# Optimization experiments

Hardware: AMD Instinct MI355X
Metric: run time of the kernel (lower is better)

The kernel has to match this reference:

```python
import jax, jax.numpy as jnp
import numpy as np

E = 1024  # embed_dim
H = 16    # num_heads
D = E // H  # head_dim
B, S = 2, 2048


def setup_inputs() -> dict:
    key = jax.random.key(0)
    ks = jax.random.split(key, 8)
    q = jax.random.normal(ks[0], (B, S, E), dtype=jnp.float32)
    k = jax.random.normal(ks[1], (B, S, E), dtype=jnp.float32)
    v = jax.random.normal(ks[2], (B, S, E), dtype=jnp.float32)
    mask = jax.random.randint(ks[3], (1, 1, S, S), 0, 2, dtype=jnp.int32)
    sc = 1.0 / np.sqrt(E)
    Wqkv = jax.random.normal(ks[4], (E, 3 * E), dtype=jnp.float32) * sc  # [in, out]
    bqkv = jnp.zeros((3 * E,), dtype=jnp.float32)
    Wout = jax.random.normal(ks[5], (E, E), dtype=jnp.float32) * sc
    bout = jnp.zeros((E,), dtype=jnp.float32)
    return {"q": q, "k": k, "v": v, "mask": mask,
            "Wqkv": Wqkv, "bqkv": bqkv, "Wout": Wout, "bout": bout}


def reference(q, k, v, mask, Wqkv, bqkv, Wout, bout):
    # Fused QKV projection: project cat([q,k,v], dim=0) with the shared 3E proj,
    # then take the Q slice for q, K slice for k, V slice for v.
    x = jnp.concatenate([q, k, v], axis=0)            # [3B, S, E]
    full = jnp.einsum('bse,ef->bsf', x, Wqkv) + bqkv  # [3B, S, 3E]
    qf, kf, vf = jnp.split(full, 3, axis=0)           # each [B, S, 3E]
    qh = qf[..., :E].reshape(B, S, H, D).transpose(0, 2, 1, 3)       # [B,H,S,D]
    kh = kf[..., E:2 * E].reshape(B, S, H, D).transpose(0, 2, 1, 3)
    vh = vf[..., 2 * E:].reshape(B, S, H, D).transpose(0, 2, 1, 3)
    scores = jnp.einsum('bhqd,bhkd->bhqk', qh, kh) / np.sqrt(D)      # [B,H,S,S]
    scores = jnp.where(mask == 0, -jnp.inf, scores)
    attn = jax.nn.softmax(scores, axis=-1)
    ctx = jnp.einsum('bhqk,bhkd->bhqd', attn, vh)                    # [B,H,S,D]
    ctx = ctx.transpose(0, 2, 1, 3).reshape(B, S, E)
    return jnp.einsum('bse,ef->bsf', ctx, Wout) + bout
```

## Files before the change

### kernel.cpp

```cpp
#include <hip/hip_runtime.h>
#include <stdint.h>

#define EDIM 1024
#define HNUM 16
#define HD   64
#define BB   2
#define SS   2048
#define MTOT (BB * SS)

typedef __attribute__((ext_vector_type(8))) __bf16 bf16x8;
typedef __attribute__((ext_vector_type(8))) short short8;
typedef __attribute__((ext_vector_type(4))) short short4v;
typedef __attribute__((ext_vector_type(4))) float f32x4;

__device__ __forceinline__ short bfbits(float f) {
  __bf16 h = (__bf16)f;
  return __builtin_bit_cast(short, h);
}

__device__ __forceinline__ void gload16(const void* g, void* l) {
  __builtin_amdgcn_global_load_lds((const __attribute__((address_space(1))) void*)g,
                                   (__attribute__((address_space(3))) void*)l, 16, 0, 0);
}

__device__ __forceinline__ int kap_perm(int k) {
  return (k & 0x20) | ((k & 0xC) << 1) | ((k & 0x10) >> 2) | (k & 3);
}

__global__ __launch_bounds__(256) void prep(
    const float* __restrict__ q, const float* __restrict__ k,
    const float* __restrict__ v, const float* __restrict__ Wqkv,
    const float* __restrict__ Wout, const int* __restrict__ mask,
    short* __restrict__ Qb, short* __restrict__ Kb, short* __restrict__ Vb,
    short* __restrict__ WqT, short* __restrict__ WkT, short* __restrict__ WvT,
    short* __restrict__ WoT, unsigned long long* __restrict__ pm) {
  __shared__ short L[64][80];
  const int bid = blockIdx.x, t = threadIdx.x;

  if (bid < 6144) {
    const int which = bid >> 11;
    const int i = (bid & 2047) * 256 + t;
    const float* s = which == 0 ? q : (which == 1 ? k : v);
    short* d = which == 0 ? Qb : (which == 1 ? Kb : Vb);
    const float4* sp = (const float4*)s + (size_t)i * 2;
    float4 a = sp[0], b = sp[1];
    short8 r;
    r[0] = bfbits(a.x); r[1] = bfbits(a.y); r[2] = bfbits(a.z); r[3] = bfbits(a.w);
    r[4] = bfbits(b.x); r[5] = bfbits(b.y); r[6] = bfbits(b.z); r[7] = bfbits(b.w);
    *(short8*)(d + (size_t)i * 8) = r;
  } else if (bid < 7168) {
    const int tb = bid - 6144;
    const int which = tb >> 8;
    const int k0 = ((tb >> 4) & 15) * 64, n0 = (tb & 15) * 64;
    const float* W = which == 3 ? Wout : Wqkv;
    const int ld = which == 3 ? EDIM : 3 * EDIM;
    const int col0 = which == 3 ? 0 : which * EDIM;
    short* D = which == 0 ? WqT : (which == 1 ? WkT : (which == 2 ? WvT : WoT));
    {
      const int kr = t >> 2, nc0 = (t & 3) * 16;
      #pragma unroll
      for (int u = 0; u < 4; ++u) {
        float4 f = *(const float4*)(W + (size_t)(k0 + kr) * ld + col0 + n0 + nc0 + u * 4);
        L[nc0 + u * 4 + 0][kr] = bfbits(f.x);
        L[nc0 + u * 4 + 1][kr] = bfbits(f.y);
        L[nc0 + u * 4 + 2][kr] = bfbits(f.z);
        L[nc0 + u * 4 + 3][kr] = bfbits(f.w);
      }
    }
    __syncthreads();
    {
      const int nr = t >> 2, kc = (t & 3) * 16;
      #pragma unroll
      for (int u = 0; u < 2; ++u) {
        short8 vv = *(const short8*)&L[nr][kc + u * 8];
        *(short8*)(D + (size_t)(n0 + nr) * EDIM + k0 + kc + u * 8) = vv;
      }
    }
  } else {
    const int wid = (bid - 7168) * 4 + (t >> 6);
    const int lane = t & 63;
    const int qq = wid >> 5, kt = wid & 31;
    const int m = mask[(size_t)qq * SS + kt * 64 + lane];
    const unsigned long long b = __ballot(m != 0);
    if (lane == 0) pm[(size_t)qq * 32 + kt] = b;
  }
}

template <int NFR, int MODE, typename OT>
__device__ __forceinline__ void gemm_body(
    const short* __restrict__ A, const short* __restrict__ Bt,
    const float* __restrict__ bias, OT* __restrict__ O,
    int m0, int n0, int K, int N, float scale, short* As, short* Bs) {
  const int t = threadIdx.x;
  const int w = t >> 6, l = t & 63;
  const int wr = w >> 1, wc = w & 1;
  const int lr4 = l >> 4, lc = l & 15;

  f32x4 acc[4][NFR] = {};
  const int srow = t >> 3;
  const int schunk = (t & 7) ^ (srow & 7);

  for (int k0 = 0; k0 < K; k0 += 64) {
    #pragma unroll
    for (int p = 0; p < 4; ++p)
      gload16(A + (size_t)(m0 + 32 * p + srow) * K + k0 + schunk * 8,
              As + p * 2048 + w * 512);
    #pragma unroll
    for (int p = 0; p < NFR; ++p)
      gload16(Bt + (size_t)(n0 + 32 * p + srow) * K + k0 + schunk * 8,
              Bs + p * 2048 + w * 512);
    __syncthreads();

    #pragma unroll
    for (int kf = 0; kf < 2; ++kf) {
      const int c = ((4 * kf + lr4) ^ (lc & 7)) * 8;
      bf16x8 a[4], bfr[NFR];
      #pragma unroll
      for (int i = 0; i < 4; ++i)
        a[i] = *(const bf16x8*)(As + (64 * wr + 16 * i + lc) * 64 + c);
      #pragma unroll
      for (int j = 0; j < NFR; ++j)
        bfr[j] = *(const bf16x8*)(Bs + (16 * NFR * wc + 16 * j + lc) * 64 + c);
      #pragma unroll
      for (int i = 0; i < 4; ++i)
        #pragma unroll
        for (int j = 0; j < NFR; ++j)
          acc[i][j] = __builtin_amdgcn_mfma_f32_16x16x32_bf16(a[i], bfr[j], acc[i][j], 0, 0, 0);
    }
    __syncthreads();
  }

  #pragma unroll
  for (int j = 0; j < NFR; ++j) {
    const int col = n0 + 16 * NFR * wc + 16 * j + lc;
    const float bv = bias[col];
    #pragma unroll
    for (int i = 0; i < 4; ++i) {
      const int rbase = m0 + 64 * wr + 16 * i + 4 * lr4;
      if constexpr (MODE == 2) {
        const int bidx = rbase >> 11, s = rbase & 2047;
        const int hh = col >> 6, dd = col & 63;
        short4v o;
        #pragma unroll
        for (int r = 0; r < 4; ++r) o[r] = bfbits((acc[i][j][r] + bv) * scale);
        *(short4v*)((short*)O + (((size_t)bidx * HNUM + hh) * 64 + dd) * SS +
                    (s & ~63) + kap_perm(s & 63)) = o;
      } else {
        #pragma unroll
        for (int r = 0; r < 4; ++r) {
          float vv = (acc[i][j][r] + bv) * scale;
          if constexpr (MODE == 0)
            ((short*)O)[(size_t)(rbase + r) * N + col] = bfbits(vv);
          else
            ((float*)O)[(size_t)(rbase + r) * N + col] = vv;
        }
      }
    }
  }
}

__global__ __launch_bounds__(256) void gemm_qkv(
    const short* __restrict__ Qb, const short* __restrict__ Kb,
    const short* __restrict__ Vb, const short* __restrict__ WqT,
    const short* __restrict__ WkT, const short* __restrict__ WvT,
    const float* __restrict__ bqkv, short* __restrict__ Qpj,
    short* __restrict__ Kpj, short* __restrict__ VT) {
  __shared__ short As[128 * 64];
  __shared__ short Bs[128 * 64];
  const int sel = blockIdx.y >> 3;
  const int n0 = (blockIdx.y & 7) * 128;
  const int m0 = blockIdx.x * 128;
  if (sel == 0)
    gemm_body<4, 0, short>(Qb, WqT, bqkv, Qpj, m0, n0, EDIM, EDIM,
                           0.125f * 1.44269504089f, As, Bs);
  else if (sel == 1)
    gemm_body<4, 0, short>(Kb, WkT, bqkv + EDIM, Kpj, m0, n0, EDIM, EDIM,
                           1.0f, As, Bs);
  else
    gemm_body<4, 2, short>(Vb, WvT, bqkv + 2 * EDIM, VT, m0, n0, EDIM, EDIM,
                           1.0f, As, Bs);
}

__global__ __launch_bounds__(256) void gemm_out(
    const short* __restrict__ A, const short* __restrict__ Bt,
    const float* __restrict__ bias, float* __restrict__ O) {
  __shared__ short As[128 * 64];
  __shared__ short Bs[64 * 64];
  gemm_body<2, 1, float>(A, Bt, bias, O, blockIdx.x * 128, blockIdx.y * 64,
                         EDIM, EDIM, 1.0f, As, Bs);
}

__global__ __launch_bounds__(256) void attn_mfma(
    const short* __restrict__ Qp, const short* __restrict__ Kp,
    const short* __restrict__ VT, const unsigned long long* __restrict__ pmask,
    short* __restrict__ Ctx) {
  __shared__ short Ks[2][64 * 64];
  __shared__ short Vt[2][64 * 64];

  const int t = threadIdx.x, w = t >> 6, l = t & 63;
  const int lr4 = l >> 4, lc = l & 15;
  const int q0 = blockIdx.x * 64;
  const int h = blockIdx.y, b = blockIdx.z;
  const size_t hb = (size_t)b * SS * EDIM + (size_t)h * HD;
  const size_t hv = ((size_t)b * HNUM + h) * 64 * SS;
  const int qrow = q0 + 16 * w + lc;

  bf16x8 qf[2];
  #pragma unroll
  for (int kf = 0; kf < 2; ++kf)
    qf[kf] = *(const bf16x8*)(Qp + hb + (size_t)qrow * EDIM + 32 * kf + 8 * lr4);

  const int srow = t >> 3;
  const int schunk = (t & 7) ^ (srow & 7);

  #pragma unroll
  for (int p = 0; p < 2; ++p) {
    gload16(Kp + hb + (size_t)(32 * p + srow) * EDIM + schunk * 8,
            &Ks[0][p * 2048 + w * 512]);
    gload16(VT + hv + (size_t)(32 * p + srow) * SS + schunk * 8,
            &Vt[0][p * 2048 + w * 512]);
  }
  __syncthreads();

  f32x4 accO[4] = {};
  float mrow = -1e30f, lrow = 0.f;
  const int NT = SS / 64;

  for (int kt = 0; kt < NT; ++kt) {
    const int cur = kt & 1, nxt = cur ^ 1;
    const unsigned long long pw = pmask[(size_t)qrow * NT + kt];
    if (kt + 1 < NT) {
      const size_t sK = hb + (size_t)((kt + 1) * 64) * EDIM;
      const size_t sV = hv + (size_t)((kt + 1) * 64);
      #pragma unroll
      for (int p = 0; p < 2; ++p) {
        gload16(Kp + sK + (size_t)(32 * p + srow) * EDIM + schunk * 8,
                &Ks[nxt][p * 2048 + w * 512]);
        gload16(VT + sV + (size_t)(32 * p + srow) * SS + schunk * 8,
                &Vt[nxt][p * 2048 + w * 512]);
      }
    }

    f32x4 sacc[4] = {};
    #pragma unroll
    for (int kf = 0; kf < 2; ++kf) {
      const int c = ((4 * kf + lr4) ^ (lc & 7)) * 8;
      #pragma unroll
      for (int nf = 0; nf < 4; ++nf) {
        bf16x8 kb8 = *(const bf16x8*)(&Ks[cur][(16 * nf + lc) * 64 + c]);
        sacc[nf] = __builtin_amdgcn_mfma_f32_16x16x32_bf16(kb8, qf[kf], sacc[nf], 0, 0, 0);
      }
    }

    float mt = -1e30f;
    #pragma unroll
    for (int nf = 0; nf < 4; ++nf)
      #pragma unroll
      for (int r = 0; r < 4; ++r)
        mt = fmaxf(mt, sacc[nf][r]);
    mt = fmaxf(mt, __shfl_xor(mt, 16, 64));
    mt = fmaxf(mt, __shfl_xor(mt, 32, 64));

    if (__any(mt > mrow + 7.0f)) {
      const float mn = fmaxf(mrow, mt);
      const float scl = exp2f(mrow - mn);
      mrow = mn;
      lrow *= scl;
      #pragma unroll
      for (int df = 0; df < 4; ++df)
        #pragma unroll
        for (int r = 0; r < 4; ++r)
          accO[df][r] *= scl;
    }

    float ls = 0.f;
    bf16x8 pf[2];
    #pragma unroll
    for (int nf = 0; nf < 4; ++nf) {
      const unsigned nib = (unsigned)(pw >> (16 * nf + 4 * lr4)) & 15u;
      #pragma unroll
      for (int r = 0; r < 4; ++r) {
        const float e = exp2f(sacc[nf][r] - mrow);
        const float p = (nib >> r) & 1u ? e : 0.f;
        ls += p;
        pf[nf >> 1][4 * (nf & 1) + r] = (__bf16)p;
      }
    }
    ls += __shfl_xor(ls, 16, 64);
    ls += __shfl_xor(ls, 32, 64);
    lrow += ls;

    #pragma unroll
    for (int kf = 0; kf < 2; ++kf) {
      const int c = ((4 * kf + lr4) ^ (lc & 7)) * 8;
      #pragma unroll
      for (int df = 0; df < 4; ++df) {
        bf16x8 va = *(const bf16x8*)(&Vt[cur][(16 * df + lc) * 64 + c]);
        accO[df] = __builtin_amdgcn_mfma_f32_16x16x32_bf16(va, pf[kf], accO[df], 0, 0, 0);
      }
    }
    __syncthreads();
  }

  const float inv = 1.f / lrow;
  #pragma unroll
  for (int df = 0; df < 4; ++df) {
    short4v o;
    #pragma unroll
    for (int r = 0; r < 4; ++r) o[r] = bfbits(accO[df][r] * inv);
    *(short4v*)(Ctx + hb + (size_t)qrow * EDIM + 16 * df + 4 * lr4) = o;
  }
}

extern "C" void kernel_launch(void* const* d_in, const int* in_sizes, int n_in,
                              void* d_out, int out_size, void* d_ws, size_t ws_size,
                              hipStream_t stream) {
  const float* q    = (const float*)d_in[0];
  const float* k    = (const float*)d_in[1];
  const float* v    = (const float*)d_in[2];
  const int*   mask = (const int*)d_in[3];
  const float* Wqkv = (const float*)d_in[4];
  const float* bqkv = (const float*)d_in[5];
  const float* Wout = (const float*)d_in[6];
  const float* bout = (const float*)d_in[7];
  float* out = (float*)d_out;

  const size_t mat = (size_t)MTOT * EDIM;
  const size_t wmat = (size_t)EDIM * EDIM;
  short* Qb  = (short*)d_ws;
  short* Kb  = Qb + mat;
  short* Vb  = Kb + mat;
  short* WqT = Vb + mat;
  short* WkT = WqT + wmat;
  short* WvT = WkT + wmat;
  short* WoT = WvT + wmat;
  short* Qpj = WoT + wmat;
  short* Kpj = Qpj + mat;
  short* VT  = Kpj + mat;
  short* Ctx = VT + mat;
  unsigned long long* pm = (unsigned long long*)(Ctx + mat);

  prep<<<dim3(23552), 256, 0, stream>>>(q, k, v, Wqkv, Wout, mask,
                                        Qb, Kb, Vb, WqT, WkT, WvT, WoT, pm);

  gemm_qkv<<<dim3(MTOT / 128, 24), 256, 0, stream>>>(Qb, Kb, Vb, WqT, WkT, WvT,
                                                     bqkv, Qpj, Kpj, VT);

  attn_mfma<<<dim3(SS / 64, HNUM, BB), 256, 0, stream>>>(Qpj, Kpj, VT, pm, Ctx);

  gemm_out<<<dim3(MTOT / 128, EDIM / 64), 256, 0, stream>>>(Ctx, WoT, bout, out);
}
```

Baseline: 267.8 us.

## Switch attention to 32x32x16 MFMA with two waves per block

The attention kernel moves from 16x16x32 to 32x32x16 bf16 MFMA tiles, so each wave owns 32 query rows and the block shrinks from four waves to two. The V-transpose permutation written by the QKV GEMM and the packed-mask bit indexing are reworked to match the new accumulator lane layout. The larger tiles aim to cut LDS reads and shuffle reductions per FLOP, at the cost of fewer waves per block and more registers per lane.

```diff
diff --git a/kernel.cpp b/kernel.cpp
--- a/kernel.cpp
+++ b/kernel.cpp
@@ -12,6 +12,7 @@
 typedef __attribute__((ext_vector_type(8))) short short8;
 typedef __attribute__((ext_vector_type(4))) short short4v;
 typedef __attribute__((ext_vector_type(4))) float f32x4;
+typedef __attribute__((ext_vector_type(16))) float f32x16;
 
 __device__ __forceinline__ short bfbits(float f) {
   __bf16 h = (__bf16)f;
@@ -23,8 +24,8 @@
                                    (__attribute__((address_space(3))) void*)l, 16, 0, 0);
 }
 
-__device__ __forceinline__ int kap_perm(int k) {
-  return (k & 0x20) | ((k & 0xC) << 1) | ((k & 0x10) >> 2) | (k & 3);
+__device__ __forceinline__ int sigma_perm(int k) {
+  return (k & ~0xC) | ((k & 4) << 1) | ((k & 8) >> 1);
 }
 
 __global__ __launch_bounds__(256) void prep(
@@ -144,7 +145,7 @@
         #pragma unroll
         for (int r = 0; r < 4; ++r) o[r] = bfbits((acc[i][j][r] + bv) * scale);
         *(short4v*)((short*)O + (((size_t)bidx * HNUM + hh) * 64 + dd) * SS +
-                    (s & ~63) + kap_perm(s & 63)) = o;
+                    (s & ~63) + sigma_perm(s & 63)) = o;
       } else {
         #pragma unroll
         for (int r = 0; r < 4; ++r) {
@@ -190,75 +191,82 @@
                          EDIM, EDIM, 1.0f, As, Bs);
 }
 
-__global__ __launch_bounds__(256) void attn_mfma(
+__global__ __launch_bounds__(128) void attn_mfma(
     const short* __restrict__ Qp, const short* __restrict__ Kp,
     const short* __restrict__ VT, const unsigned long long* __restrict__ pmask,
     short* __restrict__ Ctx) {
-  __shared__ short Ks[2][64 * 64];
-  __shared__ short Vt[2][64 * 64];
+  __shared__ short Ks[2][4096];
+  __shared__ short Vt[2][4096];
 
   const int t = threadIdx.x, w = t >> 6, l = t & 63;
-  const int lr4 = l >> 4, lc = l & 15;
+  const int l31 = l & 31, h32 = l >> 5;
   const int q0 = blockIdx.x * 64;
   const int h = blockIdx.y, b = blockIdx.z;
   const size_t hb = (size_t)b * SS * EDIM + (size_t)h * HD;
-  const size_t hv = ((size_t)b * HNUM + h) * 64 * SS;
-  const int qrow = q0 + 16 * w + lc;
-
-  bf16x8 qf[2];
-  #pragma unroll
-  for (int kf = 0; kf < 2; ++kf)
-    qf[kf] = *(const bf16x8*)(Qp + hb + (size_t)qrow * EDIM + 32 * kf + 8 * lr4);
-
-  const int srow = t >> 3;
-  const int schunk = (t & 7) ^ (srow & 7);
-
-  #pragma unroll
-  for (int p = 0; p < 2; ++p) {
-    gload16(Kp + hb + (size_t)(32 * p + srow) * EDIM + schunk * 8,
-            &Ks[0][p * 2048 + w * 512]);
-    gload16(VT + hv + (size_t)(32 * p + srow) * SS + schunk * 8,
-            &Vt[0][p * 2048 + w * 512]);
-  }
+  const size_t hv = ((size_t)b * HNUM + h) * (size_t)64 * SS;
+  const int qrow = q0 + 32 * w + l31;
+
+  bf16x8 qf[4];
+  #pragma unroll
+  for (int c = 0; c < 4; ++c)
+    qf[c] = *(const bf16x8*)(Qp + hb + (size_t)qrow * EDIM + 16 * c + 8 * h32);
+
+  int roff[4];
+  #pragma unroll
+  for (int c = 0; c < 4; ++c) roff[c] = ((2 * c + h32) ^ (l & 7)) * 8;
+  const int rowb = l31 * 64;
+
+  const int sr = l >> 3;
+  const int sc = (l & 7) ^ sr;
+  const short* ksrc = Kp + hb + (size_t)(32 * w + sr) * EDIM + sc * 8;
+  const short* vsrc = VT + hv + (size_t)(32 * w + sr) * SS + sc * 8;
+  const int ldst = w * 2048;
+
+  #pragma unroll
+  for (int p = 0; p < 4; ++p) {
+    gload16(ksrc + (size_t)(8 * p) * EDIM, &Ks[0][ldst + p * 512]);
+    gload16(vsrc + (size_t)(8 * p) * SS,  &Vt[0][ldst + p * 512]);
+  }
+  ksrc += (size_t)64 * EDIM;
+  vsrc += 64;
   __syncthreads();
 
-  f32x4 accO[4] = {};
+  f32x16 accO[2] = {};
   float mrow = -1e30f, lrow = 0.f;
+  const unsigned long long* pmp = pmask + (size_t)qrow * (SS / 64);
   const int NT = SS / 64;
 
   for (int kt = 0; kt < NT; ++kt) {
     const int cur = kt & 1, nxt = cur ^ 1;
-    const unsigned long long pw = pmask[(size_t)qrow * NT + kt];
+    const unsigned long long pw = pmp[kt];
     if (kt + 1 < NT) {
-      const size_t sK = hb + (size_t)((kt + 1) * 64) * EDIM;
-      const size_t sV = hv + (size_t)((kt + 1) * 64);
-      #pragma unroll
-      for (int p = 0; p < 2; ++p) {
-        gload16(Kp + sK + (size_t)(32 * p + srow) * EDIM + schunk * 8,
-                &Ks[nxt][p * 2048 + w * 512]);
-        gload16(VT + sV + (size_t)(32 * p + srow) * SS + schunk * 8,
-                &Vt[nxt][p * 2048 + w * 512]);
-      }
-    }
-
-    f32x4 sacc[4] = {};
-    #pragma unroll
-    for (int kf = 0; kf < 2; ++kf) {
-      const int c = ((4 * kf + lr4) ^ (lc & 7)) * 8;
-      #pragma unroll
-      for (int nf = 0; nf < 4; ++nf) {
-        bf16x8 kb8 = *(const bf16x8*)(&Ks[cur][(16 * nf + lc) * 64 + c]);
-        sacc[nf] = __builtin_amdgcn_mfma_f32_16x16x32_bf16(kb8, qf[kf], sacc[nf], 0, 0, 0);
-      }
-    }
-
-    float mt = -1e30f;
-    #pragma unroll
-    for (int nf = 0; nf < 4; ++nf)
-      #pragma unroll
-      for (int r = 0; r < 4; ++r)
-        mt = fmaxf(mt, sacc[nf][r]);
-    mt = fmaxf(mt, __shfl_xor(mt, 16, 64));
+      #pragma unroll
+      for (int p = 0; p < 4; ++p) {
+        gload16(ksrc + (size_t)(8 * p) * EDIM, &Ks[nxt][ldst + p * 512]);
+        gload16(vsrc + (size_t)(8 * p) * SS,  &Vt[nxt][ldst + p * 512]);
+      }
+      ksrc += (size_t)64 * EDIM;
+      vsrc += 64;
+    }
+
+    f32x16 sacc[2] = {};
+    #pragma unroll
+    for (int c = 0; c < 4; ++c) {
+      bf16x8 ka = *(const bf16x8*)(&Ks[cur][rowb + roff[c]]);
+      bf16x8 kb = *(const bf16x8*)(&Ks[cur][2048 + rowb + roff[c]]);
+      sacc[0] = __builtin_amdgcn_mfma_f32_32x32x16_bf16(ka, qf[c], sacc[0], 0, 0, 0);
+      sacc[1] = __builtin_amdgcn_mfma_f32_32x32x16_bf16(kb, qf[c], sacc[1], 0, 0, 0);
+    }
+
+    float mA = -1e30f, mB = -1e30f;
+    #pragma unroll
+    for (int T = 0; T < 2; ++T)
+      #pragma unroll
+      for (int g = 0; g < 4; ++g) {
+        mA = fmaxf(mA, fmaxf(sacc[T][4 * g + 0], sacc[T][4 * g + 1]));
+        mB = fmaxf(mB, fmaxf(sacc[T][4 * g + 2], sacc[T][4 * g + 3]));
+      }
+    float mt = fmaxf(mA, mB);
     mt = fmaxf(mt, __shfl_xor(mt, 32, 64));
 
     if (__any(mt > mrow + 7.0f)) {
@@ -267,49 +275,55 @@
       mrow = mn;
       lrow *= scl;
       #pragma unroll
-      for (int df = 0; df < 4; ++df)
+      for (int dt = 0; dt < 2; ++dt)
         #pragma unroll
-        for (int r = 0; r < 4; ++r)
-          accO[df][r] *= scl;
-    }
-
+        for (int r = 0; r < 16; ++r) accO[dt][r] *= scl;
+    }
+
+    const unsigned long long pwh = pw >> (4 * h32);
     float ls = 0.f;
-    bf16x8 pf[2];
-    #pragma unroll
-    for (int nf = 0; nf < 4; ++nf) {
-      const unsigned nib = (unsigned)(pw >> (16 * nf + 4 * lr4)) & 15u;
-      #pragma unroll
-      for (int r = 0; r < 4; ++r) {
-        const float e = exp2f(sacc[nf][r] - mrow);
-        const float p = (nib >> r) & 1u ? e : 0.f;
-        ls += p;
-        pf[nf >> 1][4 * (nf & 1) + r] = (__bf16)p;
-      }
-    }
-    ls += __shfl_xor(ls, 16, 64);
+    union { unsigned u[4]; bf16x8 v; } pk[4];
+    #pragma unroll
+    for (int kc = 0; kc < 4; ++kc) {
+      const int T = kc >> 1, rb = 8 * (kc & 1);
+      #pragma unroll
+      for (int wd = 0; wd < 4; ++wd) {
+        const int r0 = rb + 2 * wd, r1 = r0 + 1;
+        const int bit0 = 32 * T + 8 * (r0 >> 2) + (r0 & 3);
+        const int bit1 = 32 * T + 8 * (r1 >> 2) + (r1 & 3);
+        const float e0 = exp2f(sacc[T][r0] - mrow);
+        const float e1 = exp2f(sacc[T][r1] - mrow);
+        const float p0 = ((pwh >> bit0) & 1ull) ? e0 : 0.f;
+        const float p1 = ((pwh >> bit1) & 1ull) ? e1 : 0.f;
+        ls += p0 + p1;
+        const unsigned b0 = (unsigned short)__builtin_bit_cast(unsigned short, (__bf16)p0);
+        const unsigned b1 = (unsigned short)__builtin_bit_cast(unsigned short, (__bf16)p1);
+        pk[kc].u[wd] = b0 | (b1 << 16);
+      }
+    }
     ls += __shfl_xor(ls, 32, 64);
     lrow += ls;
 
     #pragma unroll
-    for (int kf = 0; kf < 2; ++kf) {
-      const int c = ((4 * kf + lr4) ^ (lc & 7)) * 8;
-      #pragma unroll
-      for (int df = 0; df < 4; ++df) {
-        bf16x8 va = *(const bf16x8*)(&Vt[cur][(16 * df + lc) * 64 + c]);
-        accO[df] = __builtin_amdgcn_mfma_f32_16x16x32_bf16(va, pf[kf], accO[df], 0, 0, 0);
-      }
+    for (int kc = 0; kc < 4; ++kc) {
+      bf16x8 va = *(const bf16x8*)(&Vt[cur][rowb + roff[kc]]);
+      bf16x8 vb = *(const bf16x8*)(&Vt[cur][2048 + rowb + roff[kc]]);
+      accO[0] = __builtin_amdgcn_mfma_f32_32x32x16_bf16(va, pk[kc].v, accO[0], 0, 0, 0);
+      accO[1] = __builtin_amdgcn_mfma_f32_32x32x16_bf16(vb, pk[kc].v, accO[1], 0, 0, 0);
     }
     __syncthreads();
   }
 
   const float inv = 1.f / lrow;
   #pragma unroll
-  for (int df = 0; df < 4; ++df) {
-    short4v o;
-    #pragma unroll
-    for (int r = 0; r < 4; ++r) o[r] = bfbits(accO[df][r] * inv);
-    *(short4v*)(Ctx + hb + (size_t)qrow * EDIM + 16 * df + 4 * lr4) = o;
-  }
+  for (int dt = 0; dt < 2; ++dt)
+    #pragma unroll
+    for (int g = 0; g < 4; ++g) {
+      short4v o;
+      #pragma unroll
+      for (int r = 0; r < 4; ++r) o[r] = bfbits(accO[dt][4 * g + r] * inv);
+      *(short4v*)(Ctx + hb + (size_t)qrow * EDIM + 32 * dt + 8 * g + 4 * h32) = o;
+    }
 }
 
 extern "C" void kernel_launch(void* const* d_in, const int* in_sizes, int n_in,
@@ -346,7 +360,7 @@
   gemm_qkv<<<dim3(MTOT / 128, 24), 256, 0, stream>>>(Qb, Kb, Vb, WqT, WkT, WvT,
                                                      bqkv, Qpj, Kpj, VT);
 
-  attn_mfma<<<dim3(SS / 64, HNUM, BB), 256, 0, stream>>>(Qpj, Kpj, VT, pm, Ctx);
+  attn_mfma<<<dim3(SS / 64, HNUM, BB), 128, 0, stream>>>(Qpj, Kpj, VT, pm, Ctx);
 
   gemm_out<<<dim3(MTOT / 128, EDIM / 64), 256, 0, stream>>>(Ctx, WoT, bout, out);
 }
```

New measurement: 292.3 us. +9.2%, slower.
